# Kernel optimization log

Measured on AMD Instinct MI355X. Metric: run time of the kernel, lower is better.

Reference implementation:

```python
import jax, jax.numpy as jnp
import numpy as np

N_NODES = 50000
N_EDGES = 800000
IN_DIM = 128
OUT_DIM = 64
K_KERNELS = 2
S_ATTEN = 2


def setup_inputs() -> dict:
    key = jax.random.key(0)
    ks = jax.random.split(key, 9)
    return {
        "x": jax.random.normal(ks[0], (N_NODES, IN_DIM), dtype=jnp.float32),
        "support_vals": jax.random.uniform(ks[1], (K_KERNELS, N_EDGES), dtype=jnp.float32),
        "atten_vals": jax.random.uniform(ks[2], (S_ATTEN, N_EDGES), dtype=jnp.float32),
        "W_transform": jax.random.normal(ks[3], (K_KERNELS, IN_DIM, OUT_DIM), dtype=jnp.float32) * 0.05,
        "w_left": jax.random.normal(ks[4], (K_KERNELS, S_ATTEN + 1, OUT_DIM), dtype=jnp.float32) * 0.05,
        "w_right": jax.random.normal(ks[5], (K_KERNELS, S_ATTEN + 1, OUT_DIM), dtype=jnp.float32) * 0.05,
        "W_residual": jax.random.normal(ks[6], (IN_DIM + OUT_DIM, OUT_DIM), dtype=jnp.float32) * 0.05,
        "edge_rows": jax.random.randint(ks[7], (N_EDGES,), 0, N_NODES, dtype=jnp.int64),
        "edge_cols": jax.random.randint(ks[8], (N_EDGES,), 0, N_NODES, dtype=jnp.int64),
    }


def reference(x, support_vals, atten_vals, W_transform, w_left, w_right, W_residual, edge_rows, edge_cols):
    # x: [N, F], edge lists: [E]; all supports share the same sparsity pattern.
    N = x.shape[0]
    K = W_transform.shape[0]
    output = jnp.zeros((N, W_transform.shape[2]), dtype=x.dtype)
    for k in range(K):
        wx = x @ W_transform[k]                       # [N, D]
        al = wx @ w_left[k].T                         # [N, S+1]
        ar = wx @ w_right[k].T                        # [N, S+1]
        # per-support edge values; support i=S uses this kernel's Cheb support
        vals = jnp.concatenate([atten_vals, support_vals[k][None, :]], axis=0)  # [S+1, E]
        # score_e = sum_i (al[row_e,i] + ar[col_e,i]) * vals[i,e]
        scores = jnp.einsum('es,se->e', al[edge_rows] + ar[edge_cols], vals)    # [E]
        # row-wise (segment) softmax over nonzeros, as tf.sparse_softmax
        m = jax.ops.segment_max(scores, edge_rows, num_segments=N)              # [N]
        ex = jnp.exp(scores - m[edge_rows])
        denom = jax.ops.segment_sum(ex, edge_rows, num_segments=N)              # [N]
        probs = ex / denom[edge_rows]                                           # [E]
        # spmm: out[r] = sum_{e: row_e=r} probs_e * wx[col_e]
        output = output + jax.ops.segment_sum(probs[:, None] * wx[edge_cols], edge_rows, num_segments=N)
    # residual projection then elu activation
    output = jnp.concatenate([x, output], axis=-1) @ W_residual
    return jax.nn.elu(output)
```

## Files before the change

kernel.cpp:

```cpp
#include <hip/hip_runtime.h>

#define N_NODES 50000
#define N_EDGES 800000
#define IN_DIM 128
#define OUT_DIM 64
#define NEG_INF (-1e30f)
#define GBLK ((N_NODES + 63) / 64)
#define BSHIFT 6
#define NBUK ((N_NODES + 63) >> 6)
#define NBUKP 784
#define EB 1024
#define PREB ((N_EDGES + EB - 1) / EB)
#define NFRAG (3 * 16 + 8)
#define STAGE_CAP 2048
#define BUKCAP 2048

typedef unsigned short ushort_t;
typedef __attribute__((ext_vector_type(8))) short short8;
typedef __attribute__((ext_vector_type(4))) float f32x4;
typedef __attribute__((ext_vector_type(2))) _Float16 half2_t;

__device__ __forceinline__ unsigned f2bf(float f) {
    unsigned u = __float_as_uint(f);
    u += 0x7fffu + ((u >> 16) & 1u);
    return u >> 16;
}
__device__ __forceinline__ unsigned rl_u(unsigned v, int i) {
    return __builtin_amdgcn_readlane(v, i);
}
__device__ __forceinline__ unsigned pack_h2(float a, float b) {
    auto h = __builtin_amdgcn_cvt_pkrtz(a, b);
    union { decltype(h) h2; unsigned u; } v; v.h2 = h; return v.u;
}
__device__ __forceinline__ float dot2u(unsigned w, unsigned p, float acc) {
    union { unsigned u; half2_t h; } wv, pv;
    wv.u = w; pv.u = p;
    return __builtin_amdgcn_fdot2(wv.h, pv.h, acc, false);
}

__global__ void wpack_kernel(const float* __restrict__ Wt,
                             const float* __restrict__ Wres,
                             ushort_t* __restrict__ Wpack) {
    int idx = blockIdx.x * 256 + threadIdx.x;
    if (idx >= NFRAG * 512) return;
    int f = idx >> 9;
    int within = idx & 511;
    int lane = within >> 3;
    int b = within & 7;
    float val;
    if (f < 48) {
        int mat = f >> 4;
        int ct = (f >> 2) & 3;
        int kc = f & 3;
        int k = kc * 32 + (lane >> 4) * 8 + b;
        int c = ct * 16 + (lane & 15);
        const float* W = (mat < 2) ? (Wt + (size_t)mat * IN_DIM * OUT_DIM) : Wres;
        val = W[(size_t)k * OUT_DIM + c];
    } else {
        int f2 = f - 48;
        int ct = f2 >> 1;
        int kc = f2 & 1;
        int k = kc * 32 + (lane >> 4) * 8 + b;
        int c = ct * 16 + (lane & 15);
        val = Wres[(size_t)(IN_DIM + k) * OUT_DIM + c];
    }
    Wpack[idx] = (ushort_t)f2bf(val);
}

__global__ __launch_bounds__(256) void gemm_kernel(
        const float* __restrict__ x,
        const ushort_t* __restrict__ Wpack,
        const float* __restrict__ wl,
        const float* __restrict__ wr,
        unsigned* __restrict__ wxi,
        float* __restrict__ xres,
        float* __restrict__ al,
        float* __restrict__ ar) {
    int wave = threadIdx.x >> 6;
    int lane = threadIdx.x & 63;
    int lr = lane & 15;
    int lg = lane >> 4;
    int row0 = blockIdx.x * 64 + wave * 16;

    int arow = row0 + lr;
    if (arow >= N_NODES) arow = N_NODES - 1;
    const float* xr = x + (size_t)arow * IN_DIM;
    short8 afrag[4];
#pragma unroll
    for (int kc = 0; kc < 4; ++kc) {
        float4 f0 = *(const float4*)(xr + kc * 32 + lg * 8);
        float4 f1 = *(const float4*)(xr + kc * 32 + lg * 8 + 4);
        short8 a;
        a[0] = (short)f2bf(f0.x); a[1] = (short)f2bf(f0.y);
        a[2] = (short)f2bf(f0.z); a[3] = (short)f2bf(f0.w);
        a[4] = (short)f2bf(f1.x); a[5] = (short)f2bf(f1.y);
        a[6] = (short)f2bf(f1.z); a[7] = (short)f2bf(f1.w);
        afrag[kc] = a;
    }

    f32x4 acc[3][4] = {};
#pragma unroll
    for (int kc = 0; kc < 4; ++kc) {
#pragma unroll
        for (int mat = 0; mat < 3; ++mat) {
#pragma unroll
            for (int ct = 0; ct < 4; ++ct) {
                short8 bfrag = *(const short8*)(
                    Wpack + (size_t)(((mat * 4 + ct) * 4 + kc) << 9) + lane * 8);
                acc[mat][ct] = __builtin_amdgcn_mfma_f32_16x16x32_bf16(
                    afrag[kc], bfrag, acc[mat][ct], 0, 0, 0);
            }
        }
    }

#pragma unroll
    for (int r = 0; r < 4; ++r) {
        int gr = row0 + lg * 4 + r;
        if (gr < N_NODES) {
#pragma unroll
            for (int ct = 0; ct < 4; ++ct) {
                wxi[(size_t)gr * OUT_DIM + ct * 16 + lr] =
                    pack_h2(acc[0][ct][r], acc[1][ct][r]);
                xres[(size_t)gr * OUT_DIM + ct * 16 + lr] = acc[2][ct][r];
            }
        }
    }

#pragma unroll
    for (int mat = 0; mat < 2; ++mat) {
#pragma unroll
        for (int s = 0; s < 3; ++s) {
            float wlv[4], wrv[4];
#pragma unroll
            for (int ct = 0; ct < 4; ++ct) {
                wlv[ct] = wl[(size_t)(mat * 3 + s) * OUT_DIM + ct * 16 + lr];
                wrv[ct] = wr[(size_t)(mat * 3 + s) * OUT_DIM + ct * 16 + lr];
            }
#pragma unroll
            for (int r = 0; r < 4; ++r) {
                float pl = 0.f, pr = 0.f;
#pragma unroll
                for (int ct = 0; ct < 4; ++ct) {
                    pl = fmaf(acc[mat][ct][r], wlv[ct], pl);
                    pr = fmaf(acc[mat][ct][r], wrv[ct], pr);
                }
#pragma unroll
                for (int off = 1; off < 16; off <<= 1) {
                    pl += __shfl_xor(pl, off);
                    pr += __shfl_xor(pr, off);
                }
                if (lr == 0) {
                    int gr = row0 + lg * 4 + r;
                    if (gr < N_NODES) {
                        al[(size_t)gr * 6 + mat * 3 + s] = pl;
                        ar[(size_t)gr * 6 + mat * 3 + s] = pr;
                    }
                }
            }
        }
    }
}

__global__ __launch_bounds__(256) void score_sort_kernel(
        const int* __restrict__ rows,
        const int* __restrict__ cols,
        const float* __restrict__ atten,
        const float* __restrict__ support,
        const float* __restrict__ al,
        const float* __restrict__ ar,
        uint4* __restrict__ etmp,
        uint2* __restrict__ cl) {
    __shared__ int cnt[1024];
    __shared__ int cur[1024];
    __shared__ int aux[256];
    __shared__ uint4 stage[EB];
    int t = threadIdx.x;
    cnt[t] = 0; cnt[t + 256] = 0; cnt[t + 512] = 0; cnt[t + 768] = 0;
    __syncthreads();
    int base0 = blockIdx.x * EB;
    int nval = min(EB, N_EDGES - base0);

    int r_[4], c_[4];
    float s0_[4], s1_[4];
#pragma unroll
    for (int i = 0; i < 4; ++i) {
        int e = base0 + i * 256 + t;
        bool v = e < N_EDGES;
        int r = v ? rows[e] : -1;
        int c = v ? cols[e] : 0;
        float sc0 = 0.f, sc1 = 0.f;
        if (v) {
            float a0 = atten[e], a1 = atten[N_EDGES + e];
            float sp0 = support[e], sp1 = support[N_EDGES + e];
            const float* A = al + (size_t)r * 6;
            const float* B = ar + (size_t)c * 6;
            sc0 = (A[0] + B[0]) * a0 + (A[1] + B[1]) * a1 + (A[2] + B[2]) * sp0;
            sc1 = (A[3] + B[3]) * a0 + (A[4] + B[4]) * a1 + (A[5] + B[5]) * sp1;
            atomicAdd(&cnt[r >> BSHIFT], 1);
        }
        r_[i] = r; c_[i] = c; s0_[i] = sc0; s1_[i] = sc1;
    }
    __syncthreads();
    int v0 = cnt[4 * t], v1 = cnt[4 * t + 1], v2 = cnt[4 * t + 2], v3 = cnt[4 * t + 3];
    int ps = v0 + v1 + v2 + v3;
    aux[t] = ps;
    __syncthreads();
    int val = ps;
    for (int off = 1; off < 256; off <<= 1) {
        int y = (t >= off) ? aux[t - off] : 0;
        __syncthreads();
        val += y; aux[t] = val;
        __syncthreads();
    }
    int e0x = val - ps;
    cur[4 * t]     = e0x;
    cur[4 * t + 1] = e0x + v0;
    cur[4 * t + 2] = e0x + v0 + v1;
    cur[4 * t + 3] = e0x + v0 + v1 + v2;
    size_t cb = (size_t)blockIdx.x * NBUKP;
    int vv[4] = {v0, v1, v2, v3};
#pragma unroll
    for (int j = 0; j < 4; ++j) {
        int idx = 4 * t + j;
        if (idx < NBUK) cl[cb + idx] = make_uint2((unsigned)vv[j], (unsigned)cur[idx]);
    }
    __syncthreads();
#pragma unroll
    for (int i = 0; i < 4; ++i) {
        if (r_[i] < 0) continue;
        int pos = atomicAdd(&cur[r_[i] >> BSHIFT], 1);
        uint4 pv;
        pv.x = (unsigned)c_[i] | ((unsigned)(r_[i] & 63) << 16);
        pv.y = __float_as_uint(s0_[i]);
        pv.z = __float_as_uint(s1_[i]);
        pv.w = 0u;
        stage[pos] = pv;
    }
    __syncthreads();
    for (int i = t; i < nval; i += 256)
        etmp[(size_t)base0 + i] = stage[i];
}

__global__ __launch_bounds__(256) void sortb_kernel(
        const uint2* __restrict__ cl,
        const uint4* __restrict__ etmp,
        uint4* __restrict__ edata,
        uint2* __restrict__ rowinfo) {
    __shared__ uint4 stage[STAGE_CAP];
    __shared__ int rpos[PREB + 2];
    __shared__ int lloff[PREB];
    __shared__ int aux[256];
    __shared__ int hist[64], rcur[64];
    int k = blockIdx.x, t = threadIdx.x;
    int base = k * BUKCAP;

    for (int b = t; b < PREB; b += 256) {
        uint2 v2 = cl[(size_t)b * NBUKP + k];
        rpos[b] = (int)v2.x;
        lloff[b] = (int)v2.y;
    }
    if (t < 64) hist[t] = 0;
    __syncthreads();
    int v[4];
    int idx4 = 4 * t;
#pragma unroll
    for (int i = 0; i < 4; ++i) v[i] = (idx4 + i < PREB) ? rpos[idx4 + i] : 0;
    __syncthreads();
    int s = 0;
#pragma unroll
    for (int i = 0; i < 4; ++i) { int tmp = v[i]; v[i] = s; s += tmp; }
    aux[t] = s;
    __syncthreads();
    int tv = s;
    for (int off = 1; off < 256; off <<= 1) {
        int y = (t >= off) ? aux[t - off] : 0;
        __syncthreads();
        tv += y; aux[t] = tv;
        __syncthreads();
    }
    int ofs = tv - s;
#pragma unroll
    for (int i = 0; i < 4; ++i)
        if (idx4 + i <= PREB) rpos[idx4 + i] = ofs + v[i];
    __syncthreads();
    int nb = rpos[PREB];

    for (int b = t; b < PREB; b += 256) {
        int s0 = rpos[b];
        int n = rpos[b + 1] - s0;
        int lo = lloff[b];
        const uint4* src = etmp + (size_t)b * EB + lo;
        for (int i = 0; i < n; ++i) {
            uint4 rec = src[i];
            int j = s0 + i;
            if (j < STAGE_CAP) stage[j] = rec;
            atomicAdd(&hist[(rec.x >> 16) & 63], 1);
        }
    }
    __syncthreads();
    int hv = (t < 64) ? hist[t] : 0;
    aux[t] = hv;
    __syncthreads();
    int hval = hv;
    for (int off = 1; off < 64; off <<= 1) {
        int y = (t >= off && t < 64) ? aux[t - off] : 0;
        __syncthreads();
        hval += y; aux[t] = hval;
        __syncthreads();
    }
    if (t < 64) {
        int start = hval - hv;
        rcur[t] = start;
        int row = (k << BSHIFT) + t;
        if (row < N_NODES)
            rowinfo[row] = make_uint2((unsigned)(base + start), (unsigned)hv);
    }
    __syncthreads();
    for (int j = t; j < nb; j += 256) {
        uint4 rec;
        if (j < STAGE_CAP) rec = stage[j];
        else {
            int lo = 0, hi = PREB - 1;
            while (lo < hi) { int mid = (lo + hi + 1) >> 1; if (rpos[mid] <= j) lo = mid; else hi = mid - 1; }
            rec = etmp[(size_t)lo * EB + lloff[lo] + (j - rpos[lo])];
        }
        int rl = (rec.x >> 16) & 63;
        int dst = atomicAdd(&rcur[rl], 1);
        if (dst < BUKCAP) edata[(size_t)base + dst] = rec;
    }
}

__global__ void attn_kernel(const uint2* __restrict__ rowinfo,
                            const uint4* __restrict__ edata,
                            const unsigned* __restrict__ wxi,
                            ushort_t* __restrict__ aacc) {
    int wid = blockIdx.x * 4 + (threadIdx.x >> 6);
    if (wid >= N_NODES) return;
    int lane = threadIdx.x & 63;
    uint2 ri = rowinfo[wid];
    int beg = (int)ri.x;
    int deg = (int)ri.y;
    float a = 0.f;

    if (deg > 0 && deg <= 64) {
        bool valid = lane < deg;
        uint4 ed = edata[valid ? beg + lane : beg];
        unsigned c = ed.x & 0xFFFFu;
        float sc0 = valid ? __uint_as_float(ed.y) : NEG_INF;
        float sc1 = valid ? __uint_as_float(ed.z) : NEG_INF;
        float m0 = sc0, m1 = sc1;
#pragma unroll
        for (int off = 32; off > 0; off >>= 1) {
            m0 = fmaxf(m0, __shfl_xor(m0, off));
            m1 = fmaxf(m1, __shfl_xor(m1, off));
        }
        float e0 = valid ? __expf(sc0 - m0) : 0.f;
        float e1 = valid ? __expf(sc1 - m1) : 0.f;
        float l0 = e0, l1 = e1;
#pragma unroll
        for (int off = 32; off > 0; off >>= 1) {
            l0 += __shfl_xor(l0, off);
            l1 += __shfl_xor(l1, off);
        }
        unsigned pp = pack_h2(e0 / l0, e1 / l1);
        float acc8[8] = {};
        int i = 0;
        for (; i + 8 <= deg; i += 8) {
            unsigned cc[8], vv[8];
#pragma unroll
            for (int j = 0; j < 8; ++j) cc[j] = rl_u(c, i + j);
#pragma unroll
            for (int j = 0; j < 8; ++j) vv[j] = wxi[(size_t)cc[j] * OUT_DIM + lane];
#pragma unroll
            for (int j = 0; j < 8; ++j)
                acc8[j] = dot2u(vv[j], rl_u(pp, i + j), acc8[j]);
        }
        for (; i < deg; ++i) {
            unsigned ci = rl_u(c, i);
            unsigned v = wxi[(size_t)ci * OUT_DIM + lane];
            acc8[0] = dot2u(v, rl_u(pp, i), acc8[0]);
        }
        a = ((acc8[0] + acc8[1]) + (acc8[2] + acc8[3]))
          + ((acc8[4] + acc8[5]) + (acc8[6] + acc8[7]));
    } else if (deg > 64) {
        int end = beg + deg;
        float m0 = NEG_INF, l0 = 0.f, m1 = NEG_INF, l1 = 0.f;
        for (int base = beg; base < end; base += 64) {
            int pos = base + lane;
            bool valid = pos < end;
            uint4 ed = edata[valid ? pos : beg];
            float sc0 = valid ? __uint_as_float(ed.y) : NEG_INF;
            float sc1 = valid ? __uint_as_float(ed.z) : NEG_INF;
            float cm0 = sc0, cm1 = sc1;
#pragma unroll
            for (int off = 32; off > 0; off >>= 1) {
                cm0 = fmaxf(cm0, __shfl_xor(cm0, off));
                cm1 = fmaxf(cm1, __shfl_xor(cm1, off));
            }
            float mn0 = fmaxf(m0, cm0), mn1 = fmaxf(m1, cm1);
            float e0 = valid ? __expf(sc0 - mn0) : 0.f;
            float e1 = valid ? __expf(sc1 - mn1) : 0.f;
#pragma unroll
            for (int off = 32; off > 0; off >>= 1) {
                e0 += __shfl_xor(e0, off);
                e1 += __shfl_xor(e1, off);
            }
            l0 = l0 * __expf(m0 - mn0) + e0;
            l1 = l1 * __expf(m1 - mn1) + e1;
            m0 = mn0; m1 = mn1;
        }
        float inv0 = 1.f / l0, inv1 = 1.f / l1;
        for (int base = beg; base < end; base += 64) {
            int pos = base + lane;
            bool valid = pos < end;
            uint4 ed = edata[valid ? pos : beg];
            unsigned c = ed.x & 0xFFFFu;
            float p0 = valid ? __expf(__uint_as_float(ed.y) - m0) * inv0 : 0.f;
            float p1 = valid ? __expf(__uint_as_float(ed.z) - m1) * inv1 : 0.f;
            unsigned pp = pack_h2(p0, p1);
            int cnt = min(64, end - base);
            for (int i = 0; i < cnt; ++i) {
                unsigned ci = rl_u(c, i);
                unsigned v = wxi[(size_t)ci * OUT_DIM + lane];
                a = dot2u(v, rl_u(pp, i), a);
            }
        }
    }
    aacc[(size_t)wid * OUT_DIM + lane] = (ushort_t)f2bf(a);
}

__global__ __launch_bounds__(256) void resid_kernel(
        const ushort_t* __restrict__ aacc,
        const float* __restrict__ xres,
        const ushort_t* __restrict__ Wpack,
        float* __restrict__ out) {
    int wave = threadIdx.x >> 6;
    int lane = threadIdx.x & 63;
    int lr = lane & 15;
    int lg = lane >> 4;
    int row0 = blockIdx.x * 64 + wave * 16;
    int arow = row0 + lr;
    if (arow >= N_NODES) arow = N_NODES - 1;
    const ushort_t* ap = aacc + (size_t)arow * OUT_DIM;
    short8 af[2];
#pragma unroll
    for (int kc = 0; kc < 2; ++kc)
        af[kc] = *(const short8*)(ap + kc * 32 + lg * 8);
    f32x4 acc4[4] = {};
#pragma unroll
    for (int kc = 0; kc < 2; ++kc) {
#pragma unroll
        for (int ct = 0; ct < 4; ++ct) {
            short8 bfrag = *(const short8*)(
                Wpack + (size_t)((48 + ct * 2 + kc) << 9) + lane * 8);
            acc4[ct] = __builtin_amdgcn_mfma_f32_16x16x32_bf16(
                af[kc], bfrag, acc4[ct], 0, 0, 0);
        }
    }
#pragma unroll
    for (int r = 0; r < 4; ++r) {
        int gr = row0 + lg * 4 + r;
        if (gr < N_NODES) {
#pragma unroll
            for (int ct = 0; ct < 4; ++ct) {
                float v = acc4[ct][r] + xres[(size_t)gr * OUT_DIM + ct * 16 + lr];
                out[(size_t)gr * OUT_DIM + ct * 16 + lr] = (v > 0.f) ? v : expm1f(v);
            }
        }
    }
}

extern "C" void kernel_launch(void* const* d_in, const int* in_sizes, int n_in,
                              void* d_out, int out_size, void* d_ws, size_t ws_size,
                              hipStream_t stream) {
    const float* x       = (const float*)d_in[0];
    const float* support = (const float*)d_in[1];
    const float* atten   = (const float*)d_in[2];
    const float* Wt      = (const float*)d_in[3];
    const float* wl      = (const float*)d_in[4];
    const float* wr      = (const float*)d_in[5];
    const float* Wres    = (const float*)d_in[6];
    const int*   rows    = (const int*)d_in[7];
    const int*   cols    = (const int*)d_in[8];
    float* out = (float*)d_out;

    unsigned* wxi   = (unsigned*)d_ws;
    float* xres     = (float*)(wxi + (size_t)N_NODES * OUT_DIM);
    float* al       = xres + (size_t)N_NODES * OUT_DIM;
    float* ar       = al + (size_t)N_NODES * 6;
    uint4* etmp     = (uint4*)(ar + (size_t)N_NODES * 6);
    uint4* edata    = etmp + (size_t)N_EDGES;
    uint2* rowinfo  = (uint2*)(edata + (size_t)NBUK * BUKCAP);
    uint2* cl       = rowinfo + N_NODES + 4;
    ushort_t* Wpack = (ushort_t*)(cl + (size_t)PREB * NBUKP);
    ushort_t* aacc  = (ushort_t*)etmp;

    wpack_kernel<<<(NFRAG * 512 + 255) / 256, 256, 0, stream>>>(Wt, Wres, Wpack);
    gemm_kernel<<<GBLK, 256, 0, stream>>>(x, Wpack, wl, wr, wxi, xres, al, ar);
    score_sort_kernel<<<PREB, 256, 0, stream>>>(
        rows, cols, atten, support, al, ar, etmp, cl);
    sortb_kernel<<<NBUK, 256, 0, stream>>>(cl, etmp, edata, rowinfo);
    attn_kernel<<<(N_NODES + 3) / 4, 256, 0, stream>>>(
        rowinfo, edata, wxi, aacc);
    resid_kernel<<<GBLK, 256, 0, stream>>>(aacc, xres, Wpack, out);
}
```

Baseline: 129.9 us.

## Fuse bucket sort with attention aggregation via shared-memory records; store residual in bf16

The second-stage bucket sort and the per-row attention/SpMM kernel are merged into one kernel per 64-row bucket. Each bucket keeps its sorted edge records in shared memory and processes its rows wave by wave, so the edata and rowinfo round trip through global memory and one launch go away. The residual projection is also stored as bf16 instead of fp32, halving that traffic at some precision cost. In exchange, the attention work is limited to 782 blocks of 4 waves each, which reduces parallelism and latency hiding. It also reads etmp twice (histogram pass, then scatter pass).

```diff
diff --git a/kernel.cpp b/kernel.cpp
--- a/kernel.cpp
+++ b/kernel.cpp
@@ -12,7 +12,6 @@
 #define EB 1024
 #define PREB ((N_EDGES + EB - 1) / EB)
 #define NFRAG (3 * 16 + 8)
-#define STAGE_CAP 2048
 #define BUKCAP 2048
 
 typedef unsigned short ushort_t;
@@ -24,6 +23,9 @@
     unsigned u = __float_as_uint(f);
     u += 0x7fffu + ((u >> 16) & 1u);
     return u >> 16;
+}
+__device__ __forceinline__ float bf2f(ushort_t h) {
+    return __uint_as_float((unsigned)h << 16);
 }
 __device__ __forceinline__ unsigned rl_u(unsigned v, int i) {
     return __builtin_amdgcn_readlane(v, i);
@@ -73,7 +75,7 @@
         const float* __restrict__ wl,
         const float* __restrict__ wr,
         unsigned* __restrict__ wxi,
-        float* __restrict__ xres,
+        ushort_t* __restrict__ xresh,
         float* __restrict__ al,
         float* __restrict__ ar) {
     int wave = threadIdx.x >> 6;
@@ -121,7 +123,8 @@
             for (int ct = 0; ct < 4; ++ct) {
                 wxi[(size_t)gr * OUT_DIM + ct * 16 + lr] =
                     pack_h2(acc[0][ct][r], acc[1][ct][r]);
-                xres[(size_t)gr * OUT_DIM + ct * 16 + lr] = acc[2][ct][r];
+                xresh[(size_t)gr * OUT_DIM + ct * 16 + lr] =
+                    (ushort_t)f2bf(acc[2][ct][r]);
             }
         }
     }
@@ -241,18 +244,17 @@
         etmp[(size_t)base0 + i] = stage[i];
 }
 
-__global__ __launch_bounds__(256) void sortb_kernel(
+__global__ __launch_bounds__(256) void bucket_attn_kernel(
         const uint2* __restrict__ cl,
         const uint4* __restrict__ etmp,
-        uint4* __restrict__ edata,
-        uint2* __restrict__ rowinfo) {
-    __shared__ uint4 stage[STAGE_CAP];
+        const unsigned* __restrict__ wxi,
+        ushort_t* __restrict__ aacc) {
+    __shared__ uint4 srec[BUKCAP];
     __shared__ int rpos[PREB + 2];
     __shared__ int lloff[PREB];
     __shared__ int aux[256];
-    __shared__ int hist[64], rcur[64];
+    __shared__ int hist[64], rstart[64], rcur[64];
     int k = blockIdx.x, t = threadIdx.x;
-    int base = k * BUKCAP;
 
     for (int b = t; b < PREB; b += 256) {
         uint2 v2 = cl[(size_t)b * NBUKP + k];
@@ -283,19 +285,12 @@
     for (int i = 0; i < 4; ++i)
         if (idx4 + i <= PREB) rpos[idx4 + i] = ofs + v[i];
     __syncthreads();
-    int nb = rpos[PREB];
 
     for (int b = t; b < PREB; b += 256) {
-        int s0 = rpos[b];
-        int n = rpos[b + 1] - s0;
-        int lo = lloff[b];
-        const uint4* src = etmp + (size_t)b * EB + lo;
-        for (int i = 0; i < n; ++i) {
-            uint4 rec = src[i];
-            int j = s0 + i;
-            if (j < STAGE_CAP) stage[j] = rec;
-            atomicAdd(&hist[(rec.x >> 16) & 63], 1);
-        }
+        int n = rpos[b + 1] - rpos[b];
+        const uint4* src = etmp + (size_t)b * EB + lloff[b];
+        for (int i = 0; i < n; ++i)
+            atomicAdd(&hist[(src[i].x >> 16) & 63], 1);
     }
     __syncthreads();
     int hv = (t < 64) ? hist[t] : 0;
@@ -309,129 +304,122 @@
         __syncthreads();
     }
     if (t < 64) {
-        int start = hval - hv;
-        rcur[t] = start;
-        int row = (k << BSHIFT) + t;
-        if (row < N_NODES)
-            rowinfo[row] = make_uint2((unsigned)(base + start), (unsigned)hv);
-    }
-    __syncthreads();
-    for (int j = t; j < nb; j += 256) {
-        uint4 rec;
-        if (j < STAGE_CAP) rec = stage[j];
-        else {
-            int lo = 0, hi = PREB - 1;
-            while (lo < hi) { int mid = (lo + hi + 1) >> 1; if (rpos[mid] <= j) lo = mid; else hi = mid - 1; }
-            rec = etmp[(size_t)lo * EB + lloff[lo] + (j - rpos[lo])];
-        }
-        int rl = (rec.x >> 16) & 63;
-        int dst = atomicAdd(&rcur[rl], 1);
-        if (dst < BUKCAP) edata[(size_t)base + dst] = rec;
-    }
-}
-
-__global__ void attn_kernel(const uint2* __restrict__ rowinfo,
-                            const uint4* __restrict__ edata,
-                            const unsigned* __restrict__ wxi,
-                            ushort_t* __restrict__ aacc) {
-    int wid = blockIdx.x * 4 + (threadIdx.x >> 6);
-    if (wid >= N_NODES) return;
-    int lane = threadIdx.x & 63;
-    uint2 ri = rowinfo[wid];
-    int beg = (int)ri.x;
-    int deg = (int)ri.y;
-    float a = 0.f;
-
-    if (deg > 0 && deg <= 64) {
-        bool valid = lane < deg;
-        uint4 ed = edata[valid ? beg + lane : beg];
-        unsigned c = ed.x & 0xFFFFu;
-        float sc0 = valid ? __uint_as_float(ed.y) : NEG_INF;
-        float sc1 = valid ? __uint_as_float(ed.z) : NEG_INF;
-        float m0 = sc0, m1 = sc1;
-#pragma unroll
-        for (int off = 32; off > 0; off >>= 1) {
-            m0 = fmaxf(m0, __shfl_xor(m0, off));
-            m1 = fmaxf(m1, __shfl_xor(m1, off));
-        }
-        float e0 = valid ? __expf(sc0 - m0) : 0.f;
-        float e1 = valid ? __expf(sc1 - m1) : 0.f;
-        float l0 = e0, l1 = e1;
-#pragma unroll
-        for (int off = 32; off > 0; off >>= 1) {
-            l0 += __shfl_xor(l0, off);
-            l1 += __shfl_xor(l1, off);
-        }
-        unsigned pp = pack_h2(e0 / l0, e1 / l1);
-        float acc8[8] = {};
-        int i = 0;
-        for (; i + 8 <= deg; i += 8) {
-            unsigned cc[8], vv[8];
-#pragma unroll
-            for (int j = 0; j < 8; ++j) cc[j] = rl_u(c, i + j);
-#pragma unroll
-            for (int j = 0; j < 8; ++j) vv[j] = wxi[(size_t)cc[j] * OUT_DIM + lane];
-#pragma unroll
-            for (int j = 0; j < 8; ++j)
-                acc8[j] = dot2u(vv[j], rl_u(pp, i + j), acc8[j]);
-        }
-        for (; i < deg; ++i) {
-            unsigned ci = rl_u(c, i);
-            unsigned v = wxi[(size_t)ci * OUT_DIM + lane];
-            acc8[0] = dot2u(v, rl_u(pp, i), acc8[0]);
-        }
-        a = ((acc8[0] + acc8[1]) + (acc8[2] + acc8[3]))
-          + ((acc8[4] + acc8[5]) + (acc8[6] + acc8[7]));
-    } else if (deg > 64) {
-        int end = beg + deg;
-        float m0 = NEG_INF, l0 = 0.f, m1 = NEG_INF, l1 = 0.f;
-        for (int base = beg; base < end; base += 64) {
-            int pos = base + lane;
-            bool valid = pos < end;
-            uint4 ed = edata[valid ? pos : beg];
+        rstart[t] = hval - hv;
+        rcur[t] = hval - hv;
+    }
+    __syncthreads();
+    for (int b = t; b < PREB; b += 256) {
+        int n = rpos[b + 1] - rpos[b];
+        const uint4* src = etmp + (size_t)b * EB + lloff[b];
+        for (int i = 0; i < n; ++i) {
+            uint4 rec = src[i];
+            int rl = (rec.x >> 16) & 63;
+            int dst = atomicAdd(&rcur[rl], 1);
+            if (dst < BUKCAP) srec[dst] = rec;
+        }
+    }
+    __syncthreads();
+
+    int wave = t >> 6;
+    int lane = t & 63;
+    for (int rr = wave; rr < 64; rr += 4) {
+        int row = (k << BSHIFT) + rr;
+        if (row >= N_NODES) continue;
+        int beg = rstart[rr];
+        int deg = hist[rr];
+        float a = 0.f;
+
+        if (deg > 0 && deg <= 64) {
+            bool valid = lane < deg;
+            uint4 ed = srec[valid ? beg + lane : beg];
+            unsigned c = ed.x & 0xFFFFu;
             float sc0 = valid ? __uint_as_float(ed.y) : NEG_INF;
             float sc1 = valid ? __uint_as_float(ed.z) : NEG_INF;
-            float cm0 = sc0, cm1 = sc1;
+            float m0 = sc0, m1 = sc1;
 #pragma unroll
             for (int off = 32; off > 0; off >>= 1) {
-                cm0 = fmaxf(cm0, __shfl_xor(cm0, off));
-                cm1 = fmaxf(cm1, __shfl_xor(cm1, off));
-            }
-            float mn0 = fmaxf(m0, cm0), mn1 = fmaxf(m1, cm1);
-            float e0 = valid ? __expf(sc0 - mn0) : 0.f;
-            float e1 = valid ? __expf(sc1 - mn1) : 0.f;
+                m0 = fmaxf(m0, __shfl_xor(m0, off));
+                m1 = fmaxf(m1, __shfl_xor(m1, off));
+            }
+            float e0 = valid ? __expf(sc0 - m0) : 0.f;
+            float e1 = valid ? __expf(sc1 - m1) : 0.f;
+            float l0 = e0, l1 = e1;
 #pragma unroll
             for (int off = 32; off > 0; off >>= 1) {
-                e0 += __shfl_xor(e0, off);
-                e1 += __shfl_xor(e1, off);
-            }
-            l0 = l0 * __expf(m0 - mn0) + e0;
-            l1 = l1 * __expf(m1 - mn1) + e1;
-            m0 = mn0; m1 = mn1;
-        }
-        float inv0 = 1.f / l0, inv1 = 1.f / l1;
-        for (int base = beg; base < end; base += 64) {
-            int pos = base + lane;
-            bool valid = pos < end;
-            uint4 ed = edata[valid ? pos : beg];
-            unsigned c = ed.x & 0xFFFFu;
-            float p0 = valid ? __expf(__uint_as_float(ed.y) - m0) * inv0 : 0.f;
-            float p1 = valid ? __expf(__uint_as_float(ed.z) - m1) * inv1 : 0.f;
-            unsigned pp = pack_h2(p0, p1);
-            int cnt = min(64, end - base);
-            for (int i = 0; i < cnt; ++i) {
+                l0 += __shfl_xor(l0, off);
+                l1 += __shfl_xor(l1, off);
+            }
+            unsigned pp = pack_h2(e0 / l0, e1 / l1);
+            float acc8[8] = {};
+            int i = 0;
+            for (; i + 8 <= deg; i += 8) {
+                unsigned cc[8], vv8[8];
+#pragma unroll
+                for (int j = 0; j < 8; ++j) cc[j] = rl_u(c, i + j);
+#pragma unroll
+                for (int j = 0; j < 8; ++j) vv8[j] = wxi[(size_t)cc[j] * OUT_DIM + lane];
+#pragma unroll
+                for (int j = 0; j < 8; ++j)
+                    acc8[j] = dot2u(vv8[j], rl_u(pp, i + j), acc8[j]);
+            }
+            for (; i < deg; ++i) {
                 unsigned ci = rl_u(c, i);
-                unsigned v = wxi[(size_t)ci * OUT_DIM + lane];
-                a = dot2u(v, rl_u(pp, i), a);
-            }
-        }
-    }
-    aacc[(size_t)wid * OUT_DIM + lane] = (ushort_t)f2bf(a);
+                unsigned vw = wxi[(size_t)ci * OUT_DIM + lane];
+                acc8[0] = dot2u(vw, rl_u(pp, i), acc8[0]);
+            }
+            a = ((acc8[0] + acc8[1]) + (acc8[2] + acc8[3]))
+              + ((acc8[4] + acc8[5]) + (acc8[6] + acc8[7]));
+        } else if (deg > 64) {
+            int end = beg + deg;
+            float m0 = NEG_INF, l0 = 0.f, m1 = NEG_INF, l1 = 0.f;
+            for (int base = beg; base < end; base += 64) {
+                int pos = base + lane;
+                bool valid = pos < end;
+                uint4 ed = srec[valid ? pos : beg];
+                float sc0 = valid ? __uint_as_float(ed.y) : NEG_INF;
+                float sc1 = valid ? __uint_as_float(ed.z) : NEG_INF;
+                float cm0 = sc0, cm1 = sc1;
+#pragma unroll
+                for (int off = 32; off > 0; off >>= 1) {
+                    cm0 = fmaxf(cm0, __shfl_xor(cm0, off));
+                    cm1 = fmaxf(cm1, __shfl_xor(cm1, off));
+                }
+                float mn0 = fmaxf(m0, cm0), mn1 = fmaxf(m1, cm1);
+                float e0 = valid ? __expf(sc0 - mn0) : 0.f;
+                float e1 = valid ? __expf(sc1 - mn1) : 0.f;
+#pragma unroll
+                for (int off = 32; off > 0; off >>= 1) {
+                    e0 += __shfl_xor(e0, off);
+                    e1 += __shfl_xor(e1, off);
+                }
+                l0 = l0 * __expf(m0 - mn0) + e0;
+                l1 = l1 * __expf(m1 - mn1) + e1;
+                m0 = mn0; m1 = mn1;
+            }
+            float inv0 = 1.f / l0, inv1 = 1.f / l1;
+            for (int base = beg; base < end; base += 64) {
+                int pos = base + lane;
+                bool valid = pos < end;
+                uint4 ed = srec[valid ? pos : beg];
+                unsigned c = ed.x & 0xFFFFu;
+                float p0 = valid ? __expf(__uint_as_float(ed.y) - m0) * inv0 : 0.f;
+                float p1 = valid ? __expf(__uint_as_float(ed.z) - m1) * inv1 : 0.f;
+                unsigned pp = pack_h2(p0, p1);
+                int cnt = min(64, end - base);
+                for (int i = 0; i < cnt; ++i) {
+                    unsigned ci = rl_u(c, i);
+                    unsigned vw = wxi[(size_t)ci * OUT_DIM + lane];
+                    a = dot2u(vw, rl_u(pp, i), a);
+                }
+            }
+        }
+        aacc[(size_t)row * OUT_DIM + lane] = (ushort_t)f2bf(a);
+    }
 }
 
 __global__ __launch_bounds__(256) void resid_kernel(
         const ushort_t* __restrict__ aacc,
-        const float* __restrict__ xres,
+        const ushort_t* __restrict__ xresh,
         const ushort_t* __restrict__ Wpack,
         float* __restrict__ out) {
     int wave = threadIdx.x >> 6;
@@ -463,7 +451,7 @@
         if (gr < N_NODES) {
 #pragma unroll
             for (int ct = 0; ct < 4; ++ct) {
-                float v = acc4[ct][r] + xres[(size_t)gr * OUT_DIM + ct * 16 + lr];
+                float v = acc4[ct][r] + bf2f(xresh[(size_t)gr * OUT_DIM + ct * 16 + lr]);
                 out[(size_t)gr * OUT_DIM + ct * 16 + lr] = (v > 0.f) ? v : expm1f(v);
             }
         }
@@ -484,23 +472,19 @@
     const int*   cols    = (const int*)d_in[8];
     float* out = (float*)d_out;
 
-    unsigned* wxi   = (unsigned*)d_ws;
-    float* xres     = (float*)(wxi + (size_t)N_NODES * OUT_DIM);
-    float* al       = xres + (size_t)N_NODES * OUT_DIM;
-    float* ar       = al + (size_t)N_NODES * 6;
-    uint4* etmp     = (uint4*)(ar + (size_t)N_NODES * 6);
-    uint4* edata    = etmp + (size_t)N_EDGES;
-    uint2* rowinfo  = (uint2*)(edata + (size_t)NBUK * BUKCAP);
-    uint2* cl       = rowinfo + N_NODES + 4;
-    ushort_t* Wpack = (ushort_t*)(cl + (size_t)PREB * NBUKP);
-    ushort_t* aacc  = (ushort_t*)etmp;
+    unsigned* wxi    = (unsigned*)d_ws;
+    ushort_t* xresh  = (ushort_t*)(wxi + (size_t)N_NODES * OUT_DIM);
+    float* al        = (float*)(xresh + (size_t)N_NODES * OUT_DIM);
+    float* ar        = al + (size_t)N_NODES * 6;
+    uint4* etmp      = (uint4*)(ar + (size_t)N_NODES * 6);
+    ushort_t* aacc   = (ushort_t*)(etmp + (size_t)N_EDGES);
+    uint2* cl        = (uint2*)(aacc + (size_t)N_NODES * OUT_DIM + 8);
+    ushort_t* Wpack  = (ushort_t*)(cl + (size_t)PREB * NBUKP);
 
     wpack_kernel<<<(NFRAG * 512 + 255) / 256, 256, 0, stream>>>(Wt, Wres, Wpack);
-    gemm_kernel<<<GBLK, 256, 0, stream>>>(x, Wpack, wl, wr, wxi, xres, al, ar);
+    gemm_kernel<<<GBLK, 256, 0, stream>>>(x, Wpack, wl, wr, wxi, xresh, al, ar);
     score_sort_kernel<<<PREB, 256, 0, stream>>>(
         rows, cols, atten, support, al, ar, etmp, cl);
-    sortb_kernel<<<NBUK, 256, 0, stream>>>(cl, etmp, edata, rowinfo);
-    attn_kernel<<<(N_NODES + 3) / 4, 256, 0, stream>>>(
-        rowinfo, edata, wxi, aacc);
-    resid_kernel<<<GBLK, 256, 0, stream>>>(aacc, xres, Wpack, out);
-}
+    bucket_attn_kernel<<<NBUK, 256, 0, stream>>>(cl, etmp, wxi, aacc);
+    resid_kernel<<<GBLK, 256, 0, stream>>>(aacc, xresh, Wpack, out);
+}
```

New measurement: 152.6 us. +17.5%, slower.
